# Kernel tuning notes

Hardware: AMD Instinct MI355X
Metric: run time of the kernel (lower is better)

The kernel has to match this reference:

```python
import jax, jax.numpy as jnp
import numpy as np

N, E, F_IN, H, D = 50000, 800000, 128, 4, 32


def setup_inputs() -> dict:
    key = jax.random.key(0)
    k1, k2, k3, k4 = jax.random.split(key, 4)
    feat = jax.random.normal(k1, (N, F_IN), dtype=jnp.float32)
    src = jax.random.randint(k2, (E,), 0, N, dtype=jnp.int64)
    dst = jax.random.randint(k3, (E,), 0, N, dtype=jnp.int64)
    # fc weight (xavier-normal-ish scale) and explicit bias
    W = jax.random.normal(k4, (F_IN, H * D), dtype=jnp.float32) * (1.0 / np.sqrt(F_IN))
    bias = jnp.zeros((H * D,), dtype=jnp.float32)
    return {"feat": feat, "src": src, "dst": dst, "W": W, "bias": bias}


def reference(feat, src, dst, W, bias):
    # fc projection, view as (N, H, D)
    ft = (feat @ W).reshape(N, H, D)
    # apply_edges u_dot_v: per-edge per-head dot product -> [E, H]
    e = jnp.einsum("ehd,ehd->eh", ft[src], ft[dst])
    # edge_softmax over incoming edges of each dst node (numerically stable)
    emax = jax.ops.segment_max(e, dst, num_segments=N)  # [N, H]
    ex = jnp.exp(e - emax[dst])
    denom = jax.ops.segment_sum(ex, dst, num_segments=N)  # [N, H]
    a = ex / denom[dst]  # [E, H]
    # update_all: u_mul_e + sum -> weighted scatter aggregation
    msg = ft[src] * a[:, :, None]  # [E, H, D]
    rst = jax.ops.segment_sum(msg, dst, num_segments=N)  # [N, H, D]
    return rst + bias.reshape(1, H, D)
```

## Files before the change

### kernel.cpp

```cpp
#include <hip/hip_runtime.h>
#include <math.h>

#define F 128
#define HEADS 4
#define DHEAD 32
#define HIST_H 128
#define CW_MAX 6592

typedef unsigned short ushort_t;
typedef __attribute__((ext_vector_type(8))) short short8;
typedef __attribute__((ext_vector_type(4))) float f32x4;

__device__ __forceinline__ ushort_t f2bf(float x) {
  unsigned u = __float_as_uint(x);
  unsigned r = u + 0x7FFFu + ((u >> 16) & 1u);
  return (ushort_t)(r >> 16);
}

__device__ __forceinline__ void unpack8(const int4& r, float* v) {
  int rr[4] = {r.x, r.y, r.z, r.w};
#pragma unroll
  for (int q = 0; q < 4; q++) {
    unsigned u = (unsigned)rr[q];
    v[2 * q] = __uint_as_float(u << 16);
    v[2 * q + 1] = __uint_as_float(u & 0xFFFF0000u);
  }
}

__global__ __launch_bounds__(256) void wprep_kernel(
    const float* __restrict__ W, ushort_t* __restrict__ whi,
    ushort_t* __restrict__ wlo) {
  int idx = blockIdx.x * 256 + threadIdx.x;
  if (idx >= 128 * 128) return;
  int j = idx & 7;
  int lane = (idx >> 3) & 63;
  int f = idx >> 9;
  int kt = f >> 3, nt = f & 7;
  int k = kt * 32 + (lane >> 4) * 8 + j;
  int n = nt * 16 + (lane & 15);
  float w = W[k * 128 + n];
  unsigned u = __float_as_uint(w);
  unsigned hb = u & 0xFFFF0000u;
  float lo = w - __uint_as_float(hb);
  whi[idx] = (ushort_t)(hb >> 16);
  wlo[idx] = f2bf(lo);
}

__global__ __launch_bounds__(256) void gemm_hist_kernel(
    const float* __restrict__ feat, const ushort_t* __restrict__ whi,
    const ushort_t* __restrict__ wlo, ushort_t* __restrict__ ftb, int N,
    const int* __restrict__ dst, ushort_t* __restrict__ partials, int cwp,
    int E, int gemmBlocks) {
  __shared__ int lh[CW_MAX];
  if ((int)blockIdx.x >= gemmBlocks) {
    const int hb = blockIdx.x - gemmBlocks;
    const int cls = hb & 7;
    const int h = hb >> 3;
    const int cw = (N + 7) >> 3;
    const int nbase = cls * cw;
    for (int j = threadIdx.x; j < cw; j += 256) lh[j] = 0;
    __syncthreads();
    const int seg = (E + HIST_H - 1) / HIST_H;
    const int e0 = h * seg;
    const int e1 = min(e0 + seg, E);
    int e = e0 + (int)threadIdx.x;
    for (; e + 768 < e1; e += 1024) {
      int d0 = dst[e];
      int d1 = dst[e + 256];
      int d2 = dst[e + 512];
      int d3 = dst[e + 768];
      if ((unsigned)(d0 - nbase) < (unsigned)cw) atomicAdd(&lh[d0 - nbase], 1);
      if ((unsigned)(d1 - nbase) < (unsigned)cw) atomicAdd(&lh[d1 - nbase], 1);
      if ((unsigned)(d2 - nbase) < (unsigned)cw) atomicAdd(&lh[d2 - nbase], 1);
      if ((unsigned)(d3 - nbase) < (unsigned)cw) atomicAdd(&lh[d3 - nbase], 1);
    }
    for (; e < e1; e += 256) {
      int d = dst[e];
      if ((unsigned)(d - nbase) < (unsigned)cw) atomicAdd(&lh[d - nbase], 1);
    }
    __syncthreads();
    ushort_t* prow = partials + (size_t)(cls * HIST_H + h) * cwp;
    for (int j = threadIdx.x; j < cw; j += 256) prow[j] = (ushort_t)lh[j];
    return;
  }
  const int t = threadIdx.x;
  const int wv = t >> 6;
  const int l = t & 63;
  const int g = l >> 4;
  const int lm = l & 15;
  const int arow = blockIdx.x * 64 + wv * 16 + lm;
  const int arowc = min(arow, N - 1);

  f32x4 acc[8];
#pragma unroll
  for (int nt = 0; nt < 8; nt++) acc[nt] = (f32x4){0.f, 0.f, 0.f, 0.f};

#pragma unroll
  for (int kt = 0; kt < 4; kt++) {
    const float* ap = feat + (size_t)arowc * F + kt * 32 + g * 8;
    float a[8];
    *(float4*)&a[0] = *(const float4*)ap;
    *(float4*)&a[4] = *(const float4*)(ap + 4);
    short8 ahi, alo;
#pragma unroll
    for (int j = 0; j < 8; j++) {
      unsigned u = __float_as_uint(a[j]);
      unsigned hb2 = u & 0xFFFF0000u;
      float lo = a[j] - __uint_as_float(hb2);
      ahi[j] = (short)(hb2 >> 16);
      alo[j] = (short)f2bf(lo);
    }
    const ushort_t* bh = whi + (size_t)(kt * 8) * 512 + l * 8;
    const ushort_t* bl = wlo + (size_t)(kt * 8) * 512 + l * 8;
#pragma unroll
    for (int nt = 0; nt < 8; nt++) {
      short8 bhi = *(const short8*)(bh + nt * 512);
      short8 blo = *(const short8*)(bl + nt * 512);
      acc[nt] =
          __builtin_amdgcn_mfma_f32_16x16x32_bf16(ahi, blo, acc[nt], 0, 0, 0);
      acc[nt] =
          __builtin_amdgcn_mfma_f32_16x16x32_bf16(alo, bhi, acc[nt], 0, 0, 0);
      acc[nt] =
          __builtin_amdgcn_mfma_f32_16x16x32_bf16(ahi, bhi, acc[nt], 0, 0, 0);
    }
  }

  const int orow0 = blockIdx.x * 64 + wv * 16 + g * 4;
#pragma unroll
  for (int reg = 0; reg < 4; reg++) {
    int orow = orow0 + reg;
    if (orow < N) {
#pragma unroll
      for (int nt = 0; nt < 8; nt++)
        ftb[(size_t)orow * F + nt * 16 + lm] = f2bf(acc[nt][reg]);
    }
  }
}

__global__ void scan_block_kernel(const ushort_t* __restrict__ partials,
                                  int cwp, int* __restrict__ offs,
                                  ushort_t* __restrict__ rel16,
                                  int* __restrict__ bsums, int N) {
  __shared__ int s[256];
  int t = threadIdx.x, i = blockIdx.x * 256 + t;
  int v = 0;
  if (i < N) {
    int cw = (N + 7) >> 3;
    int c = i / cw;
    int j = i - c * cw;
    const ushort_t* pb = partials + (size_t)c * HIST_H * cwp + j;
    ushort_t* cb = rel16 + (size_t)c * HIST_H * cwp + j;
    int run = 0;
#pragma unroll 8
    for (int h = 0; h < HIST_H; h++) {
      cb[(size_t)h * cwp] = (ushort_t)run;
      run += pb[(size_t)h * cwp];
    }
    v = run;
  }
  s[t] = v;
  __syncthreads();
  for (int d = 1; d < 256; d <<= 1) {
    int x = (t >= d) ? s[t - d] : 0;
    __syncthreads();
    s[t] += x;
    __syncthreads();
  }
  if (i < N) offs[i] = s[t] - v;
  if (t == 255) bsums[blockIdx.x] = s[255];
}

__global__ void scan_finish_kernel(int* __restrict__ offs,
                                   const int* __restrict__ bsums, int N,
                                   int E) {
  int t = threadIdx.x, b = blockIdx.x;
  int v = (t < b) ? bsums[t] : 0;
#pragma unroll
  for (int d = 32; d > 0; d >>= 1) v += __shfl_down(v, d, 64);
  __shared__ int wsum[4];
  if ((t & 63) == 0) wsum[t >> 6] = v;
  __syncthreads();
  int total = wsum[0] + wsum[1] + wsum[2] + wsum[3];
  int i = b * 256 + t;
  if (i < N) offs[i] += total;
  if (b == 0 && t == 0) offs[N] = E;
}

__global__ __launch_bounds__(256) void scatter_kernel(
    const int* __restrict__ src, const int* __restrict__ dst,
    const int* __restrict__ offs, const ushort_t* __restrict__ rel16, int cwp,
    int* __restrict__ csr, int E, int N) {
  __shared__ int lcur[CW_MAX];
  const int cls = blockIdx.x & 7;
  const int h = blockIdx.x >> 3;
  const int cw = (N + 7) >> 3;
  const int nbase = cls * cw;
  const int jmax = min(cw, N - nbase);
  const ushort_t* crow = rel16 + (size_t)(cls * HIST_H + h) * cwp;
  for (int j = threadIdx.x; j < jmax; j += 256)
    lcur[j] = offs[nbase + j] + (int)crow[j];
  __syncthreads();
  const int seg = (E + HIST_H - 1) / HIST_H;
  const int e0 = h * seg;
  const int e1 = min(e0 + seg, E);
  int e = e0 + (int)threadIdx.x;
  for (; e + 768 < e1; e += 1024) {
    int d0 = dst[e];
    int d1 = dst[e + 256];
    int d2 = dst[e + 512];
    int d3 = dst[e + 768];
    int s0 = src[e];
    int s1 = src[e + 256];
    int s2 = src[e + 512];
    int s3 = src[e + 768];
    if ((unsigned)(d0 - nbase) < (unsigned)cw)
      csr[atomicAdd(&lcur[d0 - nbase], 1)] = s0;
    if ((unsigned)(d1 - nbase) < (unsigned)cw)
      csr[atomicAdd(&lcur[d1 - nbase], 1)] = s1;
    if ((unsigned)(d2 - nbase) < (unsigned)cw)
      csr[atomicAdd(&lcur[d2 - nbase], 1)] = s2;
    if ((unsigned)(d3 - nbase) < (unsigned)cw)
      csr[atomicAdd(&lcur[d3 - nbase], 1)] = s3;
  }
  for (; e < e1; e += 256) {
    int d = dst[e];
    int sv = src[e];
    if ((unsigned)(d - nbase) < (unsigned)cw)
      csr[atomicAdd(&lcur[d - nbase], 1)] = sv;
  }
}

__global__ __launch_bounds__(256) void aggregate_kernel(
    const ushort_t* __restrict__ ftb, const int* __restrict__ offs,
    const int* __restrict__ csr, const float* __restrict__ bias,
    float* __restrict__ out, int N) {
  const int T = blockIdx.x * 256 + threadIdx.x;
  if (T >= N * 16) return;
  const int sub = T & 3;
  const int p = T >> 2;
  const int h = p & 3;
  const int n = p >> 2;
  const int dimBase = h * DHEAD + sub * 8;

  const int off = offs[n];
  const int deg = offs[n + 1] - off;

  float ftd[8];
  {
    int4 r = *(const int4*)&ftb[n * F + dimBase];
    unpack8(r, ftd);
  }

  const float LOG2E = 1.4426950408889634f;
  float m = -INFINITY, s = 0.f;
  float acc[8];
#pragma unroll
  for (int j = 0; j < 8; j++) acc[j] = 0.f;

#define PROCESS(RX)                                              \
  do {                                                           \
    float v[8];                                                  \
    unpack8(RX, v);                                              \
    float part = 0.f;                                            \
    _Pragma("unroll") for (int j = 0; j < 8; j++) part =         \
        fmaf(ftd[j], v[j], part);                                \
    part += __shfl_xor(part, 1, 4);                              \
    part += __shfl_xor(part, 2, 4);                              \
    float el = part * LOG2E;                                     \
    float mn = fmaxf(m, el);                                     \
    float scale = exp2f(m - mn);                                 \
    float w = exp2f(el - mn);                                    \
    s = fmaf(s, scale, w);                                       \
    _Pragma("unroll") for (int j = 0; j < 8; j++) acc[j] =       \
        fmaf(acc[j], scale, w * v[j]);                           \
    m = mn;                                                      \
  } while (0)

  int4 R0 = make_int4(0, 0, 0, 0), R1 = R0, R2 = R0, R3 = R0;
  if (deg > 0) {
    int dm1 = deg - 1;
    int s0 = csr[off];
    int s1 = csr[off + min(1, dm1)];
    int s2 = csr[off + min(2, dm1)];
    int s3 = csr[off + min(3, dm1)];
    R0 = *(const int4*)&ftb[s0 * F + dimBase];
    R1 = *(const int4*)&ftb[s1 * F + dimBase];
    R2 = *(const int4*)&ftb[s2 * F + dimBase];
    R3 = *(const int4*)&ftb[s3 * F + dimBase];
  }
  int i = 0;
  for (; i + 4 <= deg; i += 4) {
    int dm1 = deg - 1;
    int sa = csr[off + min(i + 4, dm1)];
    int sb = csr[off + min(i + 5, dm1)];
    int sc = csr[off + min(i + 6, dm1)];
    int sd = csr[off + min(i + 7, dm1)];
    int4 Na = *(const int4*)&ftb[sa * F + dimBase];
    int4 Nb = *(const int4*)&ftb[sb * F + dimBase];
    int4 Nc = *(const int4*)&ftb[sc * F + dimBase];
    int4 Nd = *(const int4*)&ftb[sd * F + dimBase];
    PROCESS(R0);
    PROCESS(R1);
    PROCESS(R2);
    PROCESS(R3);
    R0 = Na; R1 = Nb; R2 = Nc; R3 = Nd;
  }
  int r = deg - i;
  if (r > 0) PROCESS(R0);
  if (r > 1) PROCESS(R1);
  if (r > 2) PROCESS(R2);
#undef PROCESS

  float inv = (deg > 0) ? 1.f / s : 0.f;
  float4 b0 = *(const float4*)&bias[dimBase];
  float4 b1 = *(const float4*)&bias[dimBase + 4];
  f32x4 o0 = {acc[0] * inv + b0.x, acc[1] * inv + b0.y, acc[2] * inv + b0.z,
              acc[3] * inv + b0.w};
  f32x4 o1 = {acc[4] * inv + b1.x, acc[5] * inv + b1.y, acc[6] * inv + b1.z,
              acc[7] * inv + b1.w};
  __builtin_nontemporal_store(o0, (f32x4*)&out[n * F + dimBase]);
  __builtin_nontemporal_store(o1, (f32x4*)&out[n * F + dimBase + 4]);
}

extern "C" void kernel_launch(void* const* d_in, const int* in_sizes, int n_in,
                              void* d_out, int out_size, void* d_ws,
                              size_t ws_size, hipStream_t stream) {
  const float* feat = (const float*)d_in[0];
  const int* src = (const int*)d_in[1];
  const int* dst = (const int*)d_in[2];
  const float* W = (const float*)d_in[3];
  const float* bias = (const float*)d_in[4];
  float* out = (float*)d_out;

  const int N = in_sizes[0] / F;
  const int E = in_sizes[1];
  const int cw = (N + 7) >> 3;
  const int cwp = (cw + 31) & ~31;

  char* ws = (char*)d_ws;
  ushort_t* ftb = (ushort_t*)ws;
  size_t ftB = (size_t)N * F * sizeof(ushort_t);
  ftB = (ftB + 255) & ~(size_t)255;
  int* offs = (int*)(ws + ftB);
  int* bsums = offs + N + 1;
  int* csr = bsums + 256;
  ushort_t* whi = (ushort_t*)(csr + E);
  ushort_t* wlo = whi + 128 * 128;
  ushort_t* partials = wlo + 128 * 128;
  ushort_t* rel16 = partials + 8 * HIST_H * cwp;

  wprep_kernel<<<64, 256, 0, stream>>>(W, whi, wlo);

  int gemmBlocks = (N + 63) / 64;
  gemm_hist_kernel<<<gemmBlocks + 8 * HIST_H, 256, 0, stream>>>(
      feat, whi, wlo, ftb, N, dst, partials, cwp, E, gemmBlocks);

  int nb = (N + 255) / 256;
  scan_block_kernel<<<nb, 256, 0, stream>>>(partials, cwp, offs, rel16,
                                            bsums, N);
  scan_finish_kernel<<<nb, 256, 0, stream>>>(offs, bsums, N, E);

  scatter_kernel<<<8 * HIST_H, 256, 0, stream>>>(src, dst, offs, rel16, cwp,
                                                 csr, E, N);

  aggregate_kernel<<<(N * 16 + 255) / 256, 256, 0, stream>>>(ftb, offs, csr,
                                                             bias, out, N);
}
```

Measured before the change: 88.78 us.

## Split each node's edge list across four lane groups with online-softmax merge

The aggregate kernel now gives each destination node a full 64-lane wavefront instead of 16 lanes. Four groups of 16 lanes each take every fourth incoming edge, keeping their own running max, sum and accumulator. The partial results are merged with cross-lane shuffles using an online-softmax rescale. This raises memory-level parallelism and shortens each node's serial edge chain (average degree about 16), at the cost of four times as many threads, extra shuffle reduction work and idle lanes on low-degree nodes.

```diff
diff --git a/kernel.cpp b/kernel.cpp
--- a/kernel.cpp
+++ b/kernel.cpp
@@ -235,15 +235,29 @@
     const int* __restrict__ csr, const float* __restrict__ bias,
     float* __restrict__ out, int N) {
   const int T = blockIdx.x * 256 + threadIdx.x;
-  if (T >= N * 16) return;
-  const int sub = T & 3;
-  const int p = T >> 2;
-  const int h = p & 3;
-  const int n = p >> 2;
+  const int n = T >> 6;
+  if (n >= N) return;
+  const int l = T & 63;
+  const int g = l >> 4;
+  const int h = (l >> 2) & 3;
+  const int sub = l & 3;
   const int dimBase = h * DHEAD + sub * 8;
 
   const int off = offs[n];
   const int deg = offs[n + 1] - off;
+
+  float4 b0 = *(const float4*)&bias[dimBase];
+  float4 b1 = *(const float4*)&bias[dimBase + 4];
+
+  if (deg == 0) {
+    if (g == 0) {
+      f32x4 o0 = {b0.x, b0.y, b0.z, b0.w};
+      f32x4 o1 = {b1.x, b1.y, b1.z, b1.w};
+      __builtin_nontemporal_store(o0, (f32x4*)&out[n * F + dimBase]);
+      __builtin_nontemporal_store(o1, (f32x4*)&out[n * F + dimBase + 4]);
+    }
+    return;
+  }
 
   float ftd[8];
   {
@@ -276,25 +290,25 @@
     m = mn;                                                      \
   } while (0)
 
+  const int K = (deg > g) ? ((deg - g + 3) >> 2) : 0;
+  const int dm1 = deg - 1;
   int4 R0 = make_int4(0, 0, 0, 0), R1 = R0, R2 = R0, R3 = R0;
-  if (deg > 0) {
-    int dm1 = deg - 1;
-    int s0 = csr[off];
-    int s1 = csr[off + min(1, dm1)];
-    int s2 = csr[off + min(2, dm1)];
-    int s3 = csr[off + min(3, dm1)];
+  if (K > 0) {
+    int s0 = csr[off + g];
+    int s1 = csr[off + min(g + 4, dm1)];
+    int s2 = csr[off + min(g + 8, dm1)];
+    int s3 = csr[off + min(g + 12, dm1)];
     R0 = *(const int4*)&ftb[s0 * F + dimBase];
     R1 = *(const int4*)&ftb[s1 * F + dimBase];
     R2 = *(const int4*)&ftb[s2 * F + dimBase];
     R3 = *(const int4*)&ftb[s3 * F + dimBase];
   }
-  int i = 0;
-  for (; i + 4 <= deg; i += 4) {
-    int dm1 = deg - 1;
-    int sa = csr[off + min(i + 4, dm1)];
-    int sb = csr[off + min(i + 5, dm1)];
-    int sc = csr[off + min(i + 6, dm1)];
-    int sd = csr[off + min(i + 7, dm1)];
+  int k = 0;
+  for (; k + 4 <= K; k += 4) {
+    int sa = csr[off + min(g + 4 * (k + 4), dm1)];
+    int sb = csr[off + min(g + 4 * (k + 5), dm1)];
+    int sc = csr[off + min(g + 4 * (k + 6), dm1)];
+    int sd = csr[off + min(g + 4 * (k + 7), dm1)];
     int4 Na = *(const int4*)&ftb[sa * F + dimBase];
     int4 Nb = *(const int4*)&ftb[sb * F + dimBase];
     int4 Nc = *(const int4*)&ftb[sc * F + dimBase];
@@ -305,21 +319,34 @@
     PROCESS(R3);
     R0 = Na; R1 = Nb; R2 = Nc; R3 = Nd;
   }
-  int r = deg - i;
+  int r = K - k;
   if (r > 0) PROCESS(R0);
   if (r > 1) PROCESS(R1);
   if (r > 2) PROCESS(R2);
 #undef PROCESS
 
-  float inv = (deg > 0) ? 1.f / s : 0.f;
-  float4 b0 = *(const float4*)&bias[dimBase];
-  float4 b1 = *(const float4*)&bias[dimBase + 4];
-  f32x4 o0 = {acc[0] * inv + b0.x, acc[1] * inv + b0.y, acc[2] * inv + b0.z,
-              acc[3] * inv + b0.w};
-  f32x4 o1 = {acc[4] * inv + b1.x, acc[5] * inv + b1.y, acc[6] * inv + b1.z,
-              acc[7] * inv + b1.w};
-  __builtin_nontemporal_store(o0, (f32x4*)&out[n * F + dimBase]);
-  __builtin_nontemporal_store(o1, (f32x4*)&out[n * F + dimBase + 4]);
+  float mo = fmaxf(m, __shfl_xor(m, 16));
+  mo = fmaxf(mo, __shfl_xor(mo, 32));
+  float wg = exp2f(m - mo);
+  s *= wg;
+  s += __shfl_xor(s, 16);
+  s += __shfl_xor(s, 32);
+#pragma unroll
+  for (int j = 0; j < 8; j++) {
+    acc[j] *= wg;
+    acc[j] += __shfl_xor(acc[j], 16);
+    acc[j] += __shfl_xor(acc[j], 32);
+  }
+
+  if (g == 0) {
+    float inv = 1.f / s;
+    f32x4 o0 = {acc[0] * inv + b0.x, acc[1] * inv + b0.y, acc[2] * inv + b0.z,
+                acc[3] * inv + b0.w};
+    f32x4 o1 = {acc[4] * inv + b1.x, acc[5] * inv + b1.y, acc[6] * inv + b1.z,
+                acc[7] * inv + b1.w};
+    __builtin_nontemporal_store(o0, (f32x4*)&out[n * F + dimBase]);
+    __builtin_nontemporal_store(o1, (f32x4*)&out[n * F + dimBase + 4]);
+  }
 }
 
 extern "C" void kernel_launch(void* const* d_in, const int* in_sizes, int n_in,
@@ -363,6 +390,6 @@
   scatter_kernel<<<8 * HIST_H, 256, 0, stream>>>(src, dst, offs, rel16, cwp,
                                                  csr, E, N);
 
-  aggregate_kernel<<<(N * 16 + 255) / 256, 256, 0, stream>>>(ftb, offs, csr,
-                                                             bias, out, N);
-}
+  aggregate_kernel<<<(N + 3) / 4, 256, 0, stream>>>(ftb, offs, csr, bias, out,
+                                                    N);
+}
```

Result: slower. 98.25 us (+10.7%).
